# Performance work log

Measured on AMD Instinct MI355X. Metric: run time of the kernel, lower is better.

## Reference

```python
import jax, jax.numpy as jnp
import numpy as np
from jax import lax

EPS = 1e-5
DN = ('NCHW', 'OIHW', 'NCHW')


def setup_inputs() -> dict:
    key = jax.random.key(0)
    ks = jax.random.split(key, 16)
    B = 8192
    # uniform(0,1): every pixel nonzero => all voxels active => sparse conv == dense conv
    x = jax.random.uniform(ks[0], (B, 1, 28, 28), dtype=jnp.float32)

    def conv_params(kw, kb, c_in, c_out, k):
        scale = 1.0 / np.sqrt(c_in * k * k)
        w = jax.random.normal(kw, (c_out, c_in, k, k), dtype=jnp.float32) * scale
        b = jax.random.normal(kb, (c_out,), dtype=jnp.float32) * scale
        return w, b

    w0, b0 = conv_params(ks[1], ks[2], 1, 32, 3)
    w1, b1 = conv_params(ks[3], ks[4], 32, 64, 2)
    w2, b2 = conv_params(ks[5], ks[6], 64, 128, 2)
    # BatchNorm affine params (init: gamma=1, beta=0)
    g0, be0 = jnp.ones((32,), jnp.float32), jnp.zeros((32,), jnp.float32)
    g1, be1 = jnp.ones((64,), jnp.float32), jnp.zeros((64,), jnp.float32)
    g2, be2 = jnp.ones((128,), jnp.float32), jnp.zeros((128,), jnp.float32)
    w_fc = jax.random.normal(ks[7], (10, 128), dtype=jnp.float32) * (1.0 / np.sqrt(128))
    b_fc = jax.random.normal(ks[8], (10,), dtype=jnp.float32) * (1.0 / np.sqrt(128))
    return dict(x=x, w0=w0, b0=b0, g0=g0, be0=be0,
                w1=w1, b1=b1, g1=g1, be1=be1,
                w2=w2, b2=b2, g2=g2, be2=be2,
                w_fc=w_fc, b_fc=b_fc)


def _conv_bn_relu(x, w, b, g, be, stride, padding):
    # sparse conv on fully-active grid == dense conv
    y = lax.conv_general_dilated(x, w, (stride, stride), padding,
                                 dimension_numbers=DN)
    y = y + b[None, :, None, None]
    # BatchNorm1d over (N_active, C) == stats over batch+spatial (biased var)
    mean = jnp.mean(y, axis=(0, 2, 3))
    var = jnp.var(y, axis=(0, 2, 3))
    y = (y - mean[None, :, None, None]) * lax.rsqrt(var + EPS)[None, :, None, None]
    y = y * g[None, :, None, None] + be[None, :, None, None]
    return jax.nn.relu(y)


def reference(x, w0, b0, g0, be0, w1, b1, g1, be1, w2, b2, g2, be2, w_fc, b_fc):
    h = _conv_bn_relu(x, w0, b0, g0, be0, 1, 'SAME')    # (B,32,28,28)
    h = _conv_bn_relu(h, w1, b1, g1, be1, 2, 'VALID')   # (B,64,14,14)
    h = _conv_bn_relu(h, w2, b2, g2, be2, 2, 'VALID')   # (B,128,7,7)
    pooled = jnp.mean(h, axis=(2, 3))                    # AdaptiveAvgPool2d(1)+Flatten
    return pooled @ w_fc.T + b_fc                        # (B, n_classes)
```

## Files before the change

### kernel.cpp

```cpp
#include <hip/hip_runtime.h>
#include <hip/hip_bf16.h>

typedef __bf16 bf16x8 __attribute__((ext_vector_type(8)));
typedef float  f32x4  __attribute__((ext_vector_type(4)));

#define BSZ 8192

__global__ __launch_bounds__(256) void k_stats0(const float* __restrict__ x,
                                                float* __restrict__ part0,
                                                const float* __restrict__ w1,
                                                const float* __restrict__ w2,
                                                __bf16* __restrict__ w1b,
                                                __bf16* __restrict__ w2b) {
    __shared__ float sred[4 * 54];
    const int tid = threadIdx.x;
    {
        int t = blockIdx.x * 256 + tid;
        if (t < 8192) {
            int oc = t >> 7, k = t & 127, c = k & 31, d = k >> 5;
            w1b[t] = (__bf16)w1[oc * 128 + c * 4 + d];
        }
        if (t < 32768) {
            int oc = t >> 8, k = t & 255, c = k & 63, d = k >> 6;
            w2b[t] = (__bf16)w2[oc * 256 + c * 4 + d];
        }
    }
    float a[54];
#pragma unroll
    for (int i = 0; i < 54; i++) a[i] = 0.f;
    const int total = BSZ * 784;
    for (int p = blockIdx.x * 256 + tid; p < total; p += gridDim.x * 256) {
        int b = p / 784, pix = p - b * 784;
        int y = pix / 28, xx = pix - y * 28;
        const float* xb = x + (long)b * 784;
        float nv[9];
#pragma unroll
        for (int dy = 0; dy < 3; dy++) {
            int yy = y + dy - 1;
#pragma unroll
            for (int dx = 0; dx < 3; dx++) {
                int x2 = xx + dx - 1;
                nv[dy * 3 + dx] = (yy >= 0 && yy < 28 && x2 >= 0 && x2 < 28) ? xb[yy * 28 + x2] : 0.f;
            }
        }
        int idx = 0;
#pragma unroll
        for (int t2 = 0; t2 < 9; t2++) {
            float vt = nv[t2];
            a[45 + t2] += vt;
#pragma unroll
            for (int u = t2; u < 9; u++) { a[idx] += vt * nv[u]; idx++; }
        }
    }
#pragma unroll
    for (int i = 0; i < 54; i++) {
        float v = a[i];
        v += __shfl_xor(v, 1);  v += __shfl_xor(v, 2);  v += __shfl_xor(v, 4);
        v += __shfl_xor(v, 8);  v += __shfl_xor(v, 16); v += __shfl_xor(v, 32);
        a[i] = v;
    }
    const int l = tid & 63, w = tid >> 6;
    if (l == 0) {
#pragma unroll
        for (int i = 0; i < 54; i++) sred[w * 54 + i] = a[i];
    }
    __syncthreads();
    if (tid < 54)
        part0[blockIdx.x * 64 + tid] = sred[tid] + sred[54 + tid] + sred[108 + tid] + sred[162 + tid];
}

__global__ void k_fin0(const float* __restrict__ part0, const float* __restrict__ w0,
                       const float* __restrict__ g0, const float* __restrict__ be0,
                       float* __restrict__ abc0) {
    __shared__ float red[4 * 54];
    int t = threadIdx.x, c = t & 63, g = t >> 6;
    if (c < 54) {
        float acc = 0.f;
        for (int i = g; i < 1024; i += 4) acc += part0[i * 64 + c];
        red[g * 54 + c] = acc;
    }
    __syncthreads();
    if (t < 54) red[t] = red[t] + red[54 + t] + red[108 + t] + red[162 + t];
    __syncthreads();
    if (t < 32) {
        float wv[9];
#pragma unroll
        for (int tap = 0; tap < 9; tap++) wv[tap] = w0[t * 9 + tap];
        float sum = 0.f, sq = 0.f;
        int idx = 0;
#pragma unroll
        for (int ta = 0; ta < 9; ta++) {
            sum = fmaf(wv[ta], red[45 + ta], sum);
#pragma unroll
            for (int u = ta; u < 9; u++) {
                float coef = (u == ta) ? 1.f : 2.f;
                sq = fmaf(coef * wv[ta] * wv[u], red[idx], sq);
                idx++;
            }
        }
        float cnt = (float)BSZ * 784.f;
        float mean = sum / cnt;
        float var = sq / cnt - mean * mean;
        float A = g0[t] * rsqrtf(var + 1e-5f);
#pragma unroll
        for (int tap = 0; tap < 9; tap++)
            abc0[(t >> 3) * 72 + tap * 8 + (t & 7)] = A * wv[tap];
        abc0[288 + t] = be0[t] - mean * A;
    }
}

__global__ __launch_bounds__(256) void k_conv01(const float* __restrict__ x,
                                                const float* __restrict__ abc0,
                                                const __bf16* __restrict__ w1b,
                                                __bf16* __restrict__ h1,
                                                float* __restrict__ part1) {
    __shared__ float xs[30 * 30];
    __shared__ __attribute__((aligned(16))) __bf16 sAt[2][16 * 136];
    const int tid = threadIdx.x;
    if (tid < 116) {
        int idx;
        if (tid < 30)      idx = tid;
        else if (tid < 60) idx = 29 * 30 + (tid - 30);
        else if (tid < 88) idx = (tid - 60 + 1) * 30;
        else               idx = (tid - 88 + 1) * 30 + 29;
        xs[idx] = 0.f;
    }
    const int pgu = __builtin_amdgcn_readfirstlane(tid >> 6);
    const float* wfp = abc0 + pgu * 72;
    float wf[72];
#pragma unroll
    for (int i = 0; i < 72; i++) wf[i] = wfp[i];
    float c0r[8];
#pragma unroll
    for (int j = 0; j < 8; j++) c0r[j] = abc0[288 + pgu * 8 + j];

    const int pi = tid & 15, pd = (tid >> 4) & 3;
    const int w = tid >> 6, l = tid & 63, q = l >> 4, n = l & 15;
    const int oc = w * 16 + n;
    bf16x8 fbv[4];
#pragma unroll
    for (int kc = 0; kc < 4; kc++)
        fbv[kc] = *(const bf16x8*)&w1b[oc * 128 + kc * 32 + q * 8];

    for (int img = 0; img < 4; img++) {
        const int b = blockIdx.x * 4 + img;
        for (int j = tid; j < 784; j += 256) {
            int yy = j / 28, xx2 = j - yy * 28;
            xs[(yy + 1) * 30 + xx2 + 1] = x[(long)b * 784 + j];
        }
        __syncthreads();
        float ssum = 0.f, ssq = 0.f;
        __bf16* hb = h1 + (long)b * 12544 + (q * 4) * 64 + oc;
        for (int mt = 0; mt < 13; mt++) {
            __bf16* dst = &sAt[mt & 1][pi * 136 + pd * 32 + pgu * 8];
            int m = mt * 16 + pi;
            bf16x8 pk;
            if (m < 196) {
                int my = m / 14, mx = m - my * 14;
                int y0 = my * 2 + (pd >> 1), x0 = mx * 2 + (pd & 1);
                float nv[9];
#pragma unroll
                for (int dy = 0; dy < 3; dy++)
#pragma unroll
                    for (int dx = 0; dx < 3; dx++)
                        nv[dy * 3 + dx] = xs[(y0 + dy) * 30 + x0 + dx];
                float a[8];
#pragma unroll
                for (int j = 0; j < 8; j++) a[j] = c0r[j];
#pragma unroll
                for (int t = 0; t < 9; t++) {
                    float nvt = nv[t];
#pragma unroll
                    for (int j = 0; j < 8; j++) a[j] = fmaf(nvt, wf[t * 8 + j], a[j]);
                }
#pragma unroll
                for (int j = 0; j < 8; j++) pk[j] = (__bf16)fmaxf(a[j], 0.f);
            } else {
#pragma unroll
                for (int j = 0; j < 8; j++) pk[j] = (__bf16)0.0f;
            }
            *(bf16x8*)dst = pk;
            __syncthreads();
            const __bf16* sa = &sAt[mt & 1][n * 136 + q * 8];
            f32x4 acc = {0.f, 0.f, 0.f, 0.f};
#pragma unroll
            for (int kc = 0; kc < 4; kc++) {
                bf16x8 fav = *(const bf16x8*)&sa[kc * 32];
                acc = __builtin_amdgcn_mfma_f32_16x16x32_bf16(fav, fbv[kc], acc, 0, 0, 0);
            }
            bool valid = (mt < 12) | (q == 0);
            __bf16* hp = hb + mt * 16 * 64;
#pragma unroll
            for (int r = 0; r < 4; r++) {
                __bf16 hv = (__bf16)acc[r];
                if (valid) hp[r * 64] = hv;
                float fv = (float)hv;
                ssum += fv; ssq += fv * fv;
            }
        }
        ssum += __shfl_xor(ssum, 16); ssum += __shfl_xor(ssum, 32);
        ssq  += __shfl_xor(ssq, 16);  ssq  += __shfl_xor(ssq, 32);
        if (l < 16) {
            part1[(long)oc * BSZ + b] = ssum;
            part1[(long)(64 + oc) * BSZ + b] = ssq;
        }
    }
}

__global__ __launch_bounds__(256) void k_redfin(const float* __restrict__ part,
                                                const float* __restrict__ g,
                                                const float* __restrict__ be,
                                                float* __restrict__ abc,
                                                int C, float cnt) {
    __shared__ float s1[256], s2[256];
    const int c = blockIdx.x, tid = threadIdx.x;
    float a = 0.f, bq = 0.f;
    const float* p1 = part + (long)c * BSZ;
    const float* p2 = part + (long)(C + c) * BSZ;
    for (int i = tid; i < BSZ; i += 256) { a += p1[i]; bq += p2[i]; }
    s1[tid] = a; s2[tid] = bq;
    __syncthreads();
    for (int s = 128; s > 0; s >>= 1) {
        if (tid < s) { s1[tid] += s1[tid + s]; s2[tid] += s2[tid + s]; }
        __syncthreads();
    }
    if (tid == 0) {
        float mean = s1[0] / cnt;
        float var = s2[0] / cnt - mean * mean;
        float A = g[c] * rsqrtf(var + 1e-5f);
        abc[c] = A;
        abc[C + c] = be[c] - mean * A;
    }
}

__global__ __launch_bounds__(256) void k_conv2s(__bf16* __restrict__ h1,
                                                const __bf16* __restrict__ w2b,
                                                const float* __restrict__ abc1,
                                                float* __restrict__ part2) {
    __shared__ __attribute__((aligned(16))) __bf16 sAt[2][16 * 264];
    __shared__ __attribute__((aligned(16))) __bf16 zt[16 * 136];
    __shared__ float sbn1[128];
    const int tid = threadIdx.x;
    if (tid < 128) sbn1[tid] = abc1[tid];
    const int w = tid >> 6, l = tid & 63, q = l >> 4, n = l & 15;
    bf16x8 fbv[2][8];
#pragma unroll
    for (int ntl = 0; ntl < 2; ntl++) {
        int oc = (2 * w + ntl) * 16 + n;
#pragma unroll
        for (int kc = 0; kc < 8; kc++)
            fbv[ntl][kc] = *(const bf16x8*)&w2b[oc * 256 + kc * 32 + q * 8];
    }
    __syncthreads();

    for (int img = 0; img < 4; img++) {
        const int b = blockIdx.x * 4 + img;
        __bf16* src = h1 + (long)b * 12544;
        float ssum[2] = {0.f, 0.f}, ssq[2] = {0.f, 0.f};
        for (int mt = 0; mt < 4; mt++) {
#pragma unroll
            for (int it = 0; it < 2; it++) {
                int idx = it * 256 + tid;
                int rl = idx >> 5, o = (idx & 31) * 8;
                int r = mt * 16 + rl;
                bf16x8 wv;
                if (r < 49) {
                    int d = o >> 6, c = o & 63;
                    int py = r / 7, px = r - py * 7;
                    int msrc = (2 * py + (d >> 1)) * 14 + 2 * px + (d & 1);
                    bf16x8 v = *(const bf16x8*)&src[msrc * 64 + c];
#pragma unroll
                    for (int j = 0; j < 8; j++) {
                        float f = fmaxf((float)v[j] * sbn1[c + j] + sbn1[64 + c + j], 0.f);
                        wv[j] = (__bf16)f;
                    }
                } else {
#pragma unroll
                    for (int j = 0; j < 8; j++) wv[j] = (__bf16)0.0f;
                }
                *(bf16x8*)&sAt[mt & 1][rl * 264 + o] = wv;
            }
            __syncthreads();
            bf16x8 fav[8];
#pragma unroll
            for (int kc = 0; kc < 8; kc++)
                fav[kc] = *(const bf16x8*)&sAt[mt & 1][n * 264 + kc * 32 + q * 8];
#pragma unroll
            for (int ntl = 0; ntl < 2; ntl++) {
                f32x4 acc = {0.f, 0.f, 0.f, 0.f};
#pragma unroll
                for (int kc = 0; kc < 8; kc++)
                    acc = __builtin_amdgcn_mfma_f32_16x16x32_bf16(fav[kc], fbv[ntl][kc], acc, 0, 0, 0);
#pragma unroll
                for (int rr = 0; rr < 4; rr++) {
                    __bf16 hv = (__bf16)acc[rr];
                    zt[(q * 4 + rr) * 136 + (2 * w + ntl) * 16 + n] = hv;
                    float fv = (float)hv;
                    ssum[ntl] += fv; ssq[ntl] += fv * fv;
                }
            }
            __syncthreads();
            {
                int row = tid >> 4, o = (tid & 15) * 8;
                int m = mt * 16 + row;
                if (m < 49) {
                    bf16x8 zv = *(const bf16x8*)&zt[row * 136 + o];
                    *(bf16x8*)&src[m * 128 + o] = zv;
                }
            }
        }
#pragma unroll
        for (int ntl = 0; ntl < 2; ntl++) {
            ssum[ntl] += __shfl_xor(ssum[ntl], 16); ssum[ntl] += __shfl_xor(ssum[ntl], 32);
            ssq[ntl]  += __shfl_xor(ssq[ntl], 16);  ssq[ntl]  += __shfl_xor(ssq[ntl], 32);
        }
        if (l < 16) {
#pragma unroll
            for (int ntl = 0; ntl < 2; ntl++) {
                int oc = (2 * w + ntl) * 16 + l;
                part2[(long)oc * BSZ + b] = ssum[ntl];
                part2[(long)(128 + oc) * BSZ + b] = ssq[ntl];
            }
        }
    }
}

__global__ __launch_bounds__(256) void k_final(const __bf16* __restrict__ z2,
                                               const float* __restrict__ abc2,
                                               const float* __restrict__ wfc,
                                               const float* __restrict__ bfc,
                                               float* __restrict__ out) {
    __shared__ float sbn2[256];
    __shared__ float pp[16 * 128];
    __shared__ float pooled[128];
    __shared__ float fcred[80];
    const int tid = threadIdx.x;
    sbn2[tid] = abc2[tid];
    __syncthreads();
    const int g = tid & 15, c0 = g * 8, rg = tid >> 4;
    for (int img = 0; img < 4; img++) {
        const int b = blockIdx.x * 4 + img;
        const __bf16* src = z2 + (long)b * 12544;
        float acc[8];
#pragma unroll
        for (int q = 0; q < 8; q++) acc[q] = 0.f;
        for (int rr = rg; rr < 49; rr += 16) {
            bf16x8 v = *(const bf16x8*)&src[rr * 128 + c0];
#pragma unroll
            for (int q = 0; q < 8; q++) {
                float f = fmaxf((float)v[q] * sbn2[c0 + q] + sbn2[128 + c0 + q], 0.f);
                acc[q] += f;
            }
        }
        *(f32x4*)&pp[rg * 128 + c0]     = *(f32x4*)&acc[0];
        *(f32x4*)&pp[rg * 128 + c0 + 4] = *(f32x4*)&acc[4];
        __syncthreads();
        if (tid < 128) {
            float s = 0.f;
#pragma unroll
            for (int r = 0; r < 16; r++) s += pp[r * 128 + tid];
            pooled[tid] = s * (1.f / 49.f);
        }
        __syncthreads();
        if (tid < 80) {
            int o = tid >> 3, s = tid & 7;
            float a = 0.f;
#pragma unroll
            for (int j = 0; j < 16; j++) a = fmaf(pooled[s * 16 + j], wfc[o * 128 + s * 16 + j], a);
            fcred[tid] = a;
        }
        __syncthreads();
        if (tid < 10) {
            float a = bfc[tid];
#pragma unroll
            for (int s = 0; s < 8; s++) a += fcred[tid * 8 + s];
            out[(long)b * 10 + tid] = a;
        }
    }
}

extern "C" void kernel_launch(void* const* d_in, const int* in_sizes, int n_in,
                              void* d_out, int out_size, void* d_ws, size_t ws_size,
                              hipStream_t stream) {
    const float* x   = (const float*)d_in[0];
    const float* w0  = (const float*)d_in[1];
    const float* g0  = (const float*)d_in[3];
    const float* be0 = (const float*)d_in[4];
    const float* w1  = (const float*)d_in[5];
    const float* g1  = (const float*)d_in[7];
    const float* be1 = (const float*)d_in[8];
    const float* w2  = (const float*)d_in[9];
    const float* g2  = (const float*)d_in[11];
    const float* be2 = (const float*)d_in[12];
    const float* wfc = (const float*)d_in[13];
    const float* bfc = (const float*)d_in[14];
    float* out = (float*)d_out;

    float* ws    = (float*)d_ws;
    float* part0 = ws;
    float* abc0  = part0 + 1024 * 64;
    float* part1 = abc0 + 320;
    float* abc1  = part1 + 128 * BSZ;
    float* part2 = abc1 + 128;
    float* abc2  = part2 + 256 * BSZ;
    __bf16* w1b  = (__bf16*)(abc2 + 256);
    __bf16* w2b  = w1b + 8192;
    __bf16* h1   = w2b + 32768;

    k_stats0<<<dim3(1024), dim3(256), 0, stream>>>(x, part0, w1, w2, w1b, w2b);
    k_fin0<<<dim3(1), dim3(256), 0, stream>>>(part0, w0, g0, be0, abc0);
    k_conv01<<<dim3(BSZ / 4), dim3(256), 0, stream>>>(x, abc0, w1b, h1, part1);
    k_redfin<<<dim3(64), dim3(256), 0, stream>>>(part1, g1, be1, abc1, 64, (float)(BSZ * 196));
    k_conv2s<<<dim3(BSZ / 4), dim3(256), 0, stream>>>(h1, w2b, abc1, part2);
    k_redfin<<<dim3(128), dim3(256), 0, stream>>>(part2, g2, be2, abc2, 128, (float)(BSZ * 49));
    k_final<<<dim3(BSZ / 4), dim3(256), 0, stream>>>(h1, abc2, wfc, bfc, out);
}
```

Measured before the change: 410.1 us.

## Use packed float2 FMA math across kernels and double-buffer conv2 output staging

Rewrites the elementwise and stats arithmetic in the stats, conv01, conv2 and final kernels as paired f32x2 operations, so the compiler can emit packed FMA instructions (v_pk_fma_f32). The second-moment accumulators are rearranged into pairs, which changes the partial-sum layout from 54 to 59 entries. The input tile load is vectorized to float4. In conv2, the output staging buffer becomes double-buffered so the global writeback lags two tiles behind and one barrier per tile is dropped. The aim is to cut VALU instruction count and synchronisation, at the cost of more code complexity and register pressure.

```diff
diff --git a/kernel.cpp b/kernel.cpp
--- a/kernel.cpp
+++ b/kernel.cpp
@@ -3,8 +3,11 @@
 
 typedef __bf16 bf16x8 __attribute__((ext_vector_type(8)));
 typedef float  f32x4  __attribute__((ext_vector_type(4)));
+typedef float  f32x2  __attribute__((ext_vector_type(2)));
 
 #define BSZ 8192
+
+__device__ __constant__ int d_base2[9] = {0, 5, 9, 13, 16, 19, 21, 23, 24};
 
 __global__ __launch_bounds__(256) void k_stats0(const float* __restrict__ x,
                                                 float* __restrict__ part0,
@@ -12,7 +15,7 @@
                                                 const float* __restrict__ w2,
                                                 __bf16* __restrict__ w1b,
                                                 __bf16* __restrict__ w2b) {
-    __shared__ float sred[4 * 54];
+    __shared__ float sred[4 * 59];
     const int tid = threadIdx.x;
     {
         int t = blockIdx.x * 256 + tid;
@@ -25,9 +28,14 @@
             w2b[t] = (__bf16)w2[oc * 256 + c * 4 + d];
         }
     }
-    float a[54];
-#pragma unroll
-    for (int i = 0; i < 54; i++) a[i] = 0.f;
+    const int base2[9] = {0, 5, 9, 13, 16, 19, 21, 23, 24};
+    const int rsz[9]   = {5, 4, 4, 3, 3, 2, 2, 1, 1};
+    f32x2 a2[25];
+    float ax[9];
+#pragma unroll
+    for (int i = 0; i < 25; i++) a2[i] = (f32x2){0.f, 0.f};
+#pragma unroll
+    for (int i = 0; i < 9; i++) ax[i] = 0.f;
     const int total = BSZ * 784;
     for (int p = blockIdx.x * 256 + tid; p < total; p += gridDim.x * 256) {
         int b = p / 784, pix = p - b * 784;
@@ -43,59 +51,70 @@
                 nv[dy * 3 + dx] = (yy >= 0 && yy < 28 && x2 >= 0 && x2 < 28) ? xb[yy * 28 + x2] : 0.f;
             }
         }
-        int idx = 0;
-#pragma unroll
-        for (int t2 = 0; t2 < 9; t2++) {
-            float vt = nv[t2];
-            a[45 + t2] += vt;
-#pragma unroll
-            for (int u = t2; u < 9; u++) { a[idx] += vt * nv[u]; idx++; }
-        }
-    }
-#pragma unroll
-    for (int i = 0; i < 54; i++) {
-        float v = a[i];
+#pragma unroll
+        for (int t = 0; t < 9; t++) {
+            float vt = nv[t];
+            ax[t] += vt;
+            f32x2 vv = {vt, vt};
+#pragma unroll
+            for (int pp2 = 0; pp2 < 5; pp2++) {
+                if (pp2 < rsz[t]) {
+                    int u = t + 2 * pp2;
+                    f32x2 nn = {nv[u], (u + 1 < 9) ? nv[u + 1] : 0.f};
+                    a2[base2[t] + pp2] = __builtin_elementwise_fma(vv, nn, a2[base2[t] + pp2]);
+                }
+            }
+        }
+    }
+    float outv[59];
+#pragma unroll
+    for (int i = 0; i < 50; i++) outv[i] = a2[i >> 1][i & 1];
+#pragma unroll
+    for (int i = 0; i < 9; i++) outv[50 + i] = ax[i];
+#pragma unroll
+    for (int i = 0; i < 59; i++) {
+        float v = outv[i];
         v += __shfl_xor(v, 1);  v += __shfl_xor(v, 2);  v += __shfl_xor(v, 4);
         v += __shfl_xor(v, 8);  v += __shfl_xor(v, 16); v += __shfl_xor(v, 32);
-        a[i] = v;
+        outv[i] = v;
     }
     const int l = tid & 63, w = tid >> 6;
     if (l == 0) {
 #pragma unroll
-        for (int i = 0; i < 54; i++) sred[w * 54 + i] = a[i];
-    }
-    __syncthreads();
-    if (tid < 54)
-        part0[blockIdx.x * 64 + tid] = sred[tid] + sred[54 + tid] + sred[108 + tid] + sred[162 + tid];
+        for (int i = 0; i < 59; i++) sred[w * 59 + i] = outv[i];
+    }
+    __syncthreads();
+    if (tid < 59)
+        part0[blockIdx.x * 64 + tid] = sred[tid] + sred[59 + tid] + sred[118 + tid] + sred[177 + tid];
 }
 
 __global__ void k_fin0(const float* __restrict__ part0, const float* __restrict__ w0,
                        const float* __restrict__ g0, const float* __restrict__ be0,
                        float* __restrict__ abc0) {
-    __shared__ float red[4 * 54];
+    __shared__ float red[4 * 59];
     int t = threadIdx.x, c = t & 63, g = t >> 6;
-    if (c < 54) {
+    if (c < 59) {
         float acc = 0.f;
         for (int i = g; i < 1024; i += 4) acc += part0[i * 64 + c];
-        red[g * 54 + c] = acc;
-    }
-    __syncthreads();
-    if (t < 54) red[t] = red[t] + red[54 + t] + red[108 + t] + red[162 + t];
+        red[g * 59 + c] = acc;
+    }
+    __syncthreads();
+    if (t < 59) red[t] = red[t] + red[59 + t] + red[118 + t] + red[177 + t];
     __syncthreads();
     if (t < 32) {
+        const int base2[9] = {0, 5, 9, 13, 16, 19, 21, 23, 24};
         float wv[9];
 #pragma unroll
         for (int tap = 0; tap < 9; tap++) wv[tap] = w0[t * 9 + tap];
         float sum = 0.f, sq = 0.f;
-        int idx = 0;
 #pragma unroll
         for (int ta = 0; ta < 9; ta++) {
-            sum = fmaf(wv[ta], red[45 + ta], sum);
+            sum = fmaf(wv[ta], red[50 + ta], sum);
 #pragma unroll
             for (int u = ta; u < 9; u++) {
                 float coef = (u == ta) ? 1.f : 2.f;
-                sq = fmaf(coef * wv[ta] * wv[u], red[idx], sq);
-                idx++;
+                float Mv = red[2 * base2[ta] + (u - ta)];
+                sq = fmaf(coef * wv[ta] * wv[u], Mv, sq);
             }
         }
         float cnt = (float)BSZ * 784.f;
@@ -126,13 +145,14 @@
         xs[idx] = 0.f;
     }
     const int pgu = __builtin_amdgcn_readfirstlane(tid >> 6);
-    const float* wfp = abc0 + pgu * 72;
-    float wf[72];
-#pragma unroll
-    for (int i = 0; i < 72; i++) wf[i] = wfp[i];
-    float c0r[8];
-#pragma unroll
-    for (int j = 0; j < 8; j++) c0r[j] = abc0[288 + pgu * 8 + j];
+    const f32x2* wfp = (const f32x2*)(abc0 + pgu * 72);
+    f32x2 wf2[36];
+#pragma unroll
+    for (int i = 0; i < 36; i++) wf2[i] = wfp[i];
+    const f32x2* c2p = (const f32x2*)(abc0 + 288 + pgu * 8);
+    f32x2 c2[4];
+#pragma unroll
+    for (int j = 0; j < 4; j++) c2[j] = c2p[j];
 
     const int pi = tid & 15, pd = (tid >> 4) & 3;
     const int w = tid >> 6, l = tid & 63, q = l >> 4, n = l & 15;
@@ -141,15 +161,19 @@
 #pragma unroll
     for (int kc = 0; kc < 4; kc++)
         fbv[kc] = *(const bf16x8*)&w1b[oc * 128 + kc * 32 + q * 8];
+    const f32x2 zero2 = {0.f, 0.f};
 
     for (int img = 0; img < 4; img++) {
         const int b = blockIdx.x * 4 + img;
-        for (int j = tid; j < 784; j += 256) {
-            int yy = j / 28, xx2 = j - yy * 28;
-            xs[(yy + 1) * 30 + xx2 + 1] = x[(long)b * 784 + j];
-        }
-        __syncthreads();
-        float ssum = 0.f, ssq = 0.f;
+        const f32x4* xb4 = (const f32x4*)(x + (long)b * 784);
+        if (tid < 196) {
+            int yy = tid / 7, xx4 = (tid - yy * 7) * 4;
+            f32x4 v4 = xb4[tid];
+            float* dst = &xs[(yy + 1) * 30 + xx4 + 1];
+            dst[0] = v4[0]; dst[1] = v4[1]; dst[2] = v4[2]; dst[3] = v4[3];
+        }
+        __syncthreads();
+        f32x2 st_s = zero2, st_q = zero2;
         __bf16* hb = h1 + (long)b * 12544 + (q * 4) * 64 + oc;
         for (int mt = 0; mt < 13; mt++) {
             __bf16* dst = &sAt[mt & 1][pi * 136 + pd * 32 + pgu * 8];
@@ -164,17 +188,22 @@
 #pragma unroll
                     for (int dx = 0; dx < 3; dx++)
                         nv[dy * 3 + dx] = xs[(y0 + dy) * 30 + x0 + dx];
-                float a[8];
-#pragma unroll
-                for (int j = 0; j < 8; j++) a[j] = c0r[j];
+                f32x2 a2[4];
+#pragma unroll
+                for (int j = 0; j < 4; j++) a2[j] = c2[j];
 #pragma unroll
                 for (int t = 0; t < 9; t++) {
-                    float nvt = nv[t];
-#pragma unroll
-                    for (int j = 0; j < 8; j++) a[j] = fmaf(nvt, wf[t * 8 + j], a[j]);
-                }
-#pragma unroll
-                for (int j = 0; j < 8; j++) pk[j] = (__bf16)fmaxf(a[j], 0.f);
+                    f32x2 vv = {nv[t], nv[t]};
+#pragma unroll
+                    for (int j = 0; j < 4; j++)
+                        a2[j] = __builtin_elementwise_fma(vv, wf2[t * 4 + j], a2[j]);
+                }
+#pragma unroll
+                for (int j = 0; j < 4; j++) {
+                    f32x2 mv = __builtin_elementwise_max(a2[j], zero2);
+                    pk[2 * j]     = (__bf16)mv[0];
+                    pk[2 * j + 1] = (__bf16)mv[1];
+                }
             } else {
 #pragma unroll
                 for (int j = 0; j < 8; j++) pk[j] = (__bf16)0.0f;
@@ -190,14 +219,19 @@
             }
             bool valid = (mt < 12) | (q == 0);
             __bf16* hp = hb + mt * 16 * 64;
+            float fv[4];
 #pragma unroll
             for (int r = 0; r < 4; r++) {
                 __bf16 hv = (__bf16)acc[r];
                 if (valid) hp[r * 64] = hv;
-                float fv = (float)hv;
-                ssum += fv; ssq += fv * fv;
-            }
-        }
+                fv[r] = (float)hv;
+            }
+            f32x2 f01 = {fv[0], fv[1]}, f23 = {fv[2], fv[3]};
+            st_s = st_s + f01; st_s = st_s + f23;
+            st_q = __builtin_elementwise_fma(f01, f01, st_q);
+            st_q = __builtin_elementwise_fma(f23, f23, st_q);
+        }
+        float ssum = st_s[0] + st_s[1], ssq = st_q[0] + st_q[1];
         ssum += __shfl_xor(ssum, 16); ssum += __shfl_xor(ssum, 32);
         ssq  += __shfl_xor(ssq, 16);  ssq  += __shfl_xor(ssq, 32);
         if (l < 16) {
@@ -238,7 +272,7 @@
                                                 const float* __restrict__ abc1,
                                                 float* __restrict__ part2) {
     __shared__ __attribute__((aligned(16))) __bf16 sAt[2][16 * 264];
-    __shared__ __attribute__((aligned(16))) __bf16 zt[16 * 136];
+    __shared__ __attribute__((aligned(16))) __bf16 zt[2][16 * 136];
     __shared__ float sbn1[128];
     const int tid = threadIdx.x;
     if (tid < 128) sbn1[tid] = abc1[tid];
@@ -252,12 +286,28 @@
             fbv[ntl][kc] = *(const bf16x8*)&w2b[oc * 256 + kc * 32 + q * 8];
     }
     __syncthreads();
+    const int cpb = (tid & 7) * 8;
+    f32x2 A1p[4], C1p[4];
+#pragma unroll
+    for (int p = 0; p < 4; p++) {
+        A1p[p] = (f32x2){sbn1[cpb + 2 * p], sbn1[cpb + 2 * p + 1]};
+        C1p[p] = (f32x2){sbn1[64 + cpb + 2 * p], sbn1[64 + cpb + 2 * p + 1]};
+    }
+    const f32x2 zero2 = {0.f, 0.f};
+    const int srow = tid >> 4, so = (tid & 15) * 8;
 
     for (int img = 0; img < 4; img++) {
         const int b = blockIdx.x * 4 + img;
         __bf16* src = h1 + (long)b * 12544;
-        float ssum[2] = {0.f, 0.f}, ssq[2] = {0.f, 0.f};
+        f32x2 st_s[2] = {zero2, zero2}, st_q[2] = {zero2, zero2};
         for (int mt = 0; mt < 4; mt++) {
+            if (mt >= 2) {
+                int m = (mt - 2) * 16 + srow;
+                if (m < 49) {
+                    bf16x8 zv = *(const bf16x8*)&zt[mt & 1][srow * 136 + so];
+                    *(bf16x8*)&src[m * 128 + so] = zv;
+                }
+            }
 #pragma unroll
             for (int it = 0; it < 2; it++) {
                 int idx = it * 256 + tid;
@@ -265,14 +315,18 @@
                 int r = mt * 16 + rl;
                 bf16x8 wv;
                 if (r < 49) {
-                    int d = o >> 6, c = o & 63;
+                    int d = o >> 6;
+                    int c = o & 63;
                     int py = r / 7, px = r - py * 7;
                     int msrc = (2 * py + (d >> 1)) * 14 + 2 * px + (d & 1);
                     bf16x8 v = *(const bf16x8*)&src[msrc * 64 + c];
 #pragma unroll
-                    for (int j = 0; j < 8; j++) {
-                        float f = fmaxf((float)v[j] * sbn1[c + j] + sbn1[64 + c + j], 0.f);
-                        wv[j] = (__bf16)f;
+                    for (int p = 0; p < 4; p++) {
+                        f32x2 vf = {(float)v[2 * p], (float)v[2 * p + 1]};
+                        f32x2 rr = __builtin_elementwise_fma(vf, A1p[p], C1p[p]);
+                        rr = __builtin_elementwise_max(rr, zero2);
+                        wv[2 * p]     = (__bf16)rr[0];
+                        wv[2 * p + 1] = (__bf16)rr[1];
                     }
                 } else {
 #pragma unroll
@@ -291,35 +345,42 @@
 #pragma unroll
                 for (int kc = 0; kc < 8; kc++)
                     acc = __builtin_amdgcn_mfma_f32_16x16x32_bf16(fav[kc], fbv[ntl][kc], acc, 0, 0, 0);
+                float fv[4];
 #pragma unroll
                 for (int rr = 0; rr < 4; rr++) {
                     __bf16 hv = (__bf16)acc[rr];
-                    zt[(q * 4 + rr) * 136 + (2 * w + ntl) * 16 + n] = hv;
-                    float fv = (float)hv;
-                    ssum[ntl] += fv; ssq[ntl] += fv * fv;
-                }
-            }
-            __syncthreads();
-            {
-                int row = tid >> 4, o = (tid & 15) * 8;
-                int m = mt * 16 + row;
-                if (m < 49) {
-                    bf16x8 zv = *(const bf16x8*)&zt[row * 136 + o];
-                    *(bf16x8*)&src[m * 128 + o] = zv;
-                }
+                    zt[mt & 1][(q * 4 + rr) * 136 + (2 * w + ntl) * 16 + n] = hv;
+                    fv[rr] = (float)hv;
+                }
+                f32x2 f01 = {fv[0], fv[1]}, f23 = {fv[2], fv[3]};
+                st_s[ntl] = st_s[ntl] + f01; st_s[ntl] = st_s[ntl] + f23;
+                st_q[ntl] = __builtin_elementwise_fma(f01, f01, st_q[ntl]);
+                st_q[ntl] = __builtin_elementwise_fma(f23, f23, st_q[ntl]);
+            }
+        }
+        __syncthreads();
+        {
+            int m2 = 32 + srow;
+            if (m2 < 49) {
+                bf16x8 zv = *(const bf16x8*)&zt[0][srow * 136 + so];
+                *(bf16x8*)&src[m2 * 128 + so] = zv;
+            }
+            int m3 = 48 + srow;
+            if (m3 < 49) {
+                bf16x8 zv = *(const bf16x8*)&zt[1][srow * 136 + so];
+                *(bf16x8*)&src[m3 * 128 + so] = zv;
             }
         }
 #pragma unroll
         for (int ntl = 0; ntl < 2; ntl++) {
-            ssum[ntl] += __shfl_xor(ssum[ntl], 16); ssum[ntl] += __shfl_xor(ssum[ntl], 32);
-            ssq[ntl]  += __shfl_xor(ssq[ntl], 16);  ssq[ntl]  += __shfl_xor(ssq[ntl], 32);
-        }
-        if (l < 16) {
-#pragma unroll
-            for (int ntl = 0; ntl < 2; ntl++) {
+            float ssum = st_s[ntl][0] + st_s[ntl][1];
+            float ssq  = st_q[ntl][0] + st_q[ntl][1];
+            ssum += __shfl_xor(ssum, 16); ssum += __shfl_xor(ssum, 32);
+            ssq  += __shfl_xor(ssq, 16);  ssq  += __shfl_xor(ssq, 32);
+            if (l < 16) {
                 int oc = (2 * w + ntl) * 16 + l;
-                part2[(long)oc * BSZ + b] = ssum[ntl];
-                part2[(long)(128 + oc) * BSZ + b] = ssq[ntl];
+                part2[(long)oc * BSZ + b] = ssum;
+                part2[(long)(128 + oc) * BSZ + b] = ssq;
             }
         }
     }
@@ -338,22 +399,33 @@
     sbn2[tid] = abc2[tid];
     __syncthreads();
     const int g = tid & 15, c0 = g * 8, rg = tid >> 4;
+    f32x2 A2p[4], C2p[4];
+#pragma unroll
+    for (int p = 0; p < 4; p++) {
+        A2p[p] = (f32x2){sbn2[c0 + 2 * p], sbn2[c0 + 2 * p + 1]};
+        C2p[p] = (f32x2){sbn2[128 + c0 + 2 * p], sbn2[128 + c0 + 2 * p + 1]};
+    }
+    const f32x2 zero2 = {0.f, 0.f};
     for (int img = 0; img < 4; img++) {
         const int b = blockIdx.x * 4 + img;
         const __bf16* src = z2 + (long)b * 12544;
-        float acc[8];
-#pragma unroll
-        for (int q = 0; q < 8; q++) acc[q] = 0.f;
+        f32x2 acc2[4];
+#pragma unroll
+        for (int p = 0; p < 4; p++) acc2[p] = zero2;
         for (int rr = rg; rr < 49; rr += 16) {
             bf16x8 v = *(const bf16x8*)&src[rr * 128 + c0];
 #pragma unroll
-            for (int q = 0; q < 8; q++) {
-                float f = fmaxf((float)v[q] * sbn2[c0 + q] + sbn2[128 + c0 + q], 0.f);
-                acc[q] += f;
-            }
-        }
-        *(f32x4*)&pp[rg * 128 + c0]     = *(f32x4*)&acc[0];
-        *(f32x4*)&pp[rg * 128 + c0 + 4] = *(f32x4*)&acc[4];
+            for (int p = 0; p < 4; p++) {
+                f32x2 vf = {(float)v[2 * p], (float)v[2 * p + 1]};
+                f32x2 t0 = __builtin_elementwise_fma(vf, A2p[p], C2p[p]);
+                t0 = __builtin_elementwise_max(t0, zero2);
+                acc2[p] = acc2[p] + t0;
+            }
+        }
+        f32x4 lo = {acc2[0][0], acc2[0][1], acc2[1][0], acc2[1][1]};
+        f32x4 hi = {acc2[2][0], acc2[2][1], acc2[3][0], acc2[3][1]};
+        *(f32x4*)&pp[rg * 128 + c0]     = lo;
+        *(f32x4*)&pp[rg * 128 + c0 + 4] = hi;
         __syncthreads();
         if (tid < 128) {
             float s = 0.f;
```

After: 410.3 us. No clear change (+0.0%).
